# Performance work log

Hardware: AMD Instinct MI355X
Metric: run time of the kernel (lower is better)

Reference implementation:

```python
import jax, jax.numpy as jnp
import numpy as np

D_MODEL = 1024
NUM_HEADS = 16
HEAD_DIM = D_MODEL // NUM_HEADS


def setup_inputs() -> dict:
    key = jax.random.key(0)
    ks = jax.random.split(key, 5)
    scale = 1.0 / np.sqrt(D_MODEL)
    x = jax.random.normal(ks[0], (2, 2048, D_MODEL), dtype=jnp.float32)
    W_qkv = jax.random.normal(ks[1], (D_MODEL, 3 * D_MODEL), dtype=jnp.float32) * scale
    b_qkv = jnp.zeros((3 * D_MODEL,), dtype=jnp.float32)
    W_proj = jax.random.normal(ks[2], (D_MODEL, D_MODEL), dtype=jnp.float32) * scale
    b_proj = jnp.zeros((D_MODEL,), dtype=jnp.float32)
    return {"x": x, "W_qkv": W_qkv, "b_qkv": b_qkv, "W_proj": W_proj, "b_proj": b_proj}


def reference(x, W_qkv, b_qkv, W_proj, b_proj):
    B, S, D = x.shape
    qkv = x @ W_qkv + b_qkv                      # [B,S,3D]
    qkv = qkv.reshape(B, S, 3, NUM_HEADS, HEAD_DIM)
    qkv = jnp.transpose(qkv, (2, 0, 3, 1, 4))    # [3,B,H,S,hd]
    q, k, v = qkv[0], qkv[1], qkv[2]
    scores = jnp.einsum('bhqd,bhkd->bhqk', q, k) / jnp.sqrt(jnp.asarray(HEAD_DIM, x.dtype))
    probs = jax.nn.softmax(scores, axis=-1)
    out = jnp.einsum('bhqk,bhkd->bhqd', probs, v)  # [B,H,S,hd]
    out = jnp.transpose(out, (0, 2, 1, 3)).reshape(B, S, D)
    return out @ W_proj + b_proj
```

## Files before the change

kernel.cpp:

```cpp
#include <hip/hip_runtime.h>
#include <math.h>

#define B_ 2
#define S_ 2048
#define D_ 1024
#define H_ 16
#define HD_ 64

typedef __bf16 bf16x8 __attribute__((ext_vector_type(8)));
typedef __bf16 bf16x4 __attribute__((ext_vector_type(4)));
typedef __bf16 bf16x2 __attribute__((ext_vector_type(2)));
typedef float f32x4 __attribute__((ext_vector_type(4)));
typedef float f32x16 __attribute__((ext_vector_type(16)));
typedef unsigned u32x2 __attribute__((ext_vector_type(2)));

#define GLOAD16(gsrc, ldst) \
  __builtin_amdgcn_global_load_lds((const __attribute__((address_space(1))) void*)(gsrc), \
                                   (__attribute__((address_space(3))) void*)(ldst), 16, 0, 0)

static __device__ __forceinline__ unsigned pack2(float a, float b) {
    bf16x2 v; v[0] = (__bf16)a; v[1] = (__bf16)b;
    return __builtin_bit_cast(unsigned, v);
}

__global__ __launch_bounds__(256) void conv_k(
    const float* __restrict__ in, __bf16* __restrict__ out)
{
    int i = (blockIdx.x * 256 + threadIdx.x) * 8;
    float4 a = *(const float4*)(in + i);
    float4 b = *(const float4*)(in + i + 4);
    bf16x8 v;
    v[0] = (__bf16)a.x; v[1] = (__bf16)a.y; v[2] = (__bf16)a.z; v[3] = (__bf16)a.w;
    v[4] = (__bf16)b.x; v[5] = (__bf16)b.y; v[6] = (__bf16)b.z; v[7] = (__bf16)b.w;
    *(bf16x8*)(out + i) = v;
}

__global__ __launch_bounds__(256) void transpose_bf16_k(
    const float* __restrict__ in, __bf16* __restrict__ t_out, int K, int N)
{
    __shared__ float t[64][65];
    const int tid = threadIdx.x;
    const int bj = blockIdx.x * 64;
    const int bi = blockIdx.y * 64;
    #pragma unroll
    for (int it = 0; it < 4; ++it) {
        int idx = (tid + it * 256) * 4;
        int r = idx >> 6, c = idx & 63;
        float4 v = *(const float4*)(in + (size_t)(bi + r) * N + bj + c);
        t[r][c] = v.x; t[r][c+1] = v.y; t[r][c+2] = v.z; t[r][c+3] = v.w;
    }
    __syncthreads();
    int j = tid & 63;
    int i0 = (tid >> 6) * 16;
    bf16x8 h0, h1;
    #pragma unroll
    for (int ii = 0; ii < 8; ++ii) h0[ii] = (__bf16)t[i0 + ii][j];
    #pragma unroll
    for (int ii = 0; ii < 8; ++ii) h1[ii] = (__bf16)t[i0 + 8 + ii][j];
    size_t o = (size_t)(bj + j) * K + bi + i0;
    *(bf16x8*)(t_out + o) = h0; *(bf16x8*)(t_out + o + 8) = h1;
}

template<typename OutT>
__global__ __launch_bounds__(256) void gemm_nt_k(
    const __bf16* __restrict__ A, const __bf16* __restrict__ Bt,
    const float* __restrict__ bias, OutT* __restrict__ C,
    int M, int N, int K)
{
    constexpr int TSZ = 128 * 64;
    __shared__ __bf16 sA[TSZ];
    __shared__ __bf16 sB[TSZ];

    const int tid = threadIdx.x, w = tid >> 6, l = tid & 63;
    const int lr = l & 15, lg = l >> 4;
    const int bm = blockIdx.y * 128, bn = blockIdx.x * 128;
    const int wm = w >> 1, wn = w & 1;

    f32x4 acc[4][4] = {};

    for (int k0 = 0; k0 < K; k0 += 64) {
        __syncthreads();
        #pragma unroll
        for (int c = 0; c < 4; ++c) {
            int q = w * 4 + c;
            int r = q * 8 + (l >> 3);
            int sl = ((l & 7) ^ (r & 7)) * 8;
            GLOAD16(A + (size_t)(bm + r) * K + k0 + sl, sA + q * 512);
            GLOAD16(Bt + (size_t)(bn + r) * K + k0 + sl, sB + q * 512);
        }
        __syncthreads();
        #pragma unroll
        for (int kk = 0; kk < 2; ++kk) {
            bf16x8 ah[4], bh[4];
            #pragma unroll
            for (int i = 0; i < 4; ++i) {
                int ra = wm * 64 + i * 16 + lr;
                int sa = ((kk * 4 + lg) ^ (ra & 7)) * 8;
                ah[i] = *(const bf16x8*)(sA + ra * 64 + sa);
                int rb = wn * 64 + i * 16 + lr;
                int sb = ((kk * 4 + lg) ^ (rb & 7)) * 8;
                bh[i] = *(const bf16x8*)(sB + rb * 64 + sb);
            }
            #pragma unroll
            for (int mi = 0; mi < 4; ++mi)
                #pragma unroll
                for (int ni = 0; ni < 4; ++ni)
                    acc[mi][ni] = __builtin_amdgcn_mfma_f32_16x16x32_bf16(ah[mi], bh[ni], acc[mi][ni], 0, 0, 0);
        }
    }

    #pragma unroll
    for (int ni = 0; ni < 4; ++ni) {
        int col = bn + wn * 64 + ni * 16 + lr;
        float bv = bias[col];
        #pragma unroll
        for (int mi = 0; mi < 4; ++mi) {
            #pragma unroll
            for (int r = 0; r < 4; ++r) {
                int row = bm + wm * 64 + mi * 16 + lg * 4 + r;
                float v = acc[mi][ni][r] + bv;
                C[(size_t)row * N + col] = (OutT)v;
            }
        }
    }
}

__global__ __launch_bounds__(512) void attn32_k(
    const __bf16* __restrict__ qkv, __bf16* __restrict__ attn)
{
    __shared__ __bf16 Ks[2][64 * 64];
    __shared__ __bf16 Vt[2][64 * 64];

    const int tid = threadIdx.x, w = tid >> 6, l = tid & 63;
    const int q32 = l & 31, hi = l >> 5;
    const int bid = blockIdx.x;
    const int qt = bid >> 5, hb = bid & 31;
    const int h = hb >> 1, b = hb & 1;
    const int q0 = qt * 256;
    const size_t ldq = 3 * D_;
    const __bf16* Qg = qkv + (size_t)b * S_ * ldq + h * HD_;
    const __bf16* Kg = Qg + D_;
    const __bf16* Vg = Qg + 2 * D_;
    const int qg = q0 + w * 32 + q32;

    const float C2  = 0.125f * 1.44269504f;
    const float OFF = 20.0f * 1.44269504f;

    bf16x8 qf[4];
    #pragma unroll
    for (int ds = 0; ds < 4; ++ds)
        qf[ds] = *(const bf16x8*)(Qg + (size_t)qg * ldq + ds * 16 + hi * 8);

    const int krow = tid >> 3;
    const int ksl  = (tid & 7) ^ (krow & 7);
    const int vk   = tid & 63;
    const int vd0  = (tid >> 6) * 8;
    int voff[8];
    #pragma unroll
    for (int j = 0; j < 8; ++j)
        voff[j] = (vd0 + j) * 128 + (((vk >> 3) ^ j) * 16) + (vk & 7) * 2;

    f32x16 o[2] = {};
    float lsum = 0.f;
    bf16x8 vr;

    auto stageK = [&](int kt, int buf) {
        GLOAD16(Kg + (size_t)(kt * 64 + krow) * ldq + ksl * 8, &Ks[buf][w * 512]);
    };
    auto loadV = [&](int kt) {
        vr = *(const bf16x8*)(Vg + (size_t)(kt * 64 + vk) * ldq + vd0);
    };
    auto writeV = [&](int buf) {
        #pragma unroll
        for (int j = 0; j < 8; ++j)
            *(__bf16*)((char*)&Vt[buf][0] + voff[j]) = vr[j];
    };

    stageK(0, 0);
    loadV(0);
    writeV(0);
    __syncthreads();

    constexpr int NT = S_ / 64;
    for (int kt = 0; kt < NT; ++kt) {
        const int cur = kt & 1, nxt = cur ^ 1;
        if (kt < NT - 1) { stageK(kt + 1, nxt); loadV(kt + 1); }

        f32x16 sc[2] = {};
        #pragma unroll
        for (int kb = 0; kb < 2; ++kb) {
            int r = kb * 32 + q32;
            #pragma unroll
            for (int ds = 0; ds < 4; ++ds) {
                int slot = (ds * 2 + hi) ^ (r & 7);
                bf16x8 kf = *(const bf16x8*)((const char*)&Ks[cur][0] + r * 128 + slot * 16);
                sc[kb] = __builtin_amdgcn_mfma_f32_32x32x16_bf16(kf, qf[ds], sc[kb], 0, 0, 0);
            }
        }

        float sum = 0.f;
        #pragma unroll
        for (int kb = 0; kb < 2; ++kb)
            #pragma unroll
            for (int i = 0; i < 16; ++i) {
                float pv = exp2f(fmaf(sc[kb][i], C2, -OFF));
                sc[kb][i] = pv;
                sum += pv;
            }
        lsum += sum;

        bf16x8 pa[2][2];
        #pragma unroll
        for (int kb = 0; kb < 2; ++kb) {
            #pragma unroll
            for (int tl = 0; tl < 2; ++tl) {
                int base = tl * 8;
                unsigned A0 = pack2(sc[kb][base + 0], sc[kb][base + 1]);
                unsigned A1 = pack2(sc[kb][base + 2], sc[kb][base + 3]);
                unsigned B0 = pack2(sc[kb][base + 4], sc[kb][base + 5]);
                unsigned B1 = pack2(sc[kb][base + 6], sc[kb][base + 7]);
                u32x2 s0 = __builtin_amdgcn_permlane32_swap(A0, B0, false, false);
                u32x2 s1 = __builtin_amdgcn_permlane32_swap(A1, B1, false, false);
                union { unsigned u[4]; bf16x8 v; } pu;
                pu.u[0] = s0[0]; pu.u[1] = s1[0]; pu.u[2] = s0[1]; pu.u[3] = s1[1];
                pa[kb][tl] = pu.v;
            }
        }

        #pragma unroll
        for (int db = 0; db < 2; ++db) {
            int dr = db * 32 + q32;
            #pragma unroll
            for (int t = 0; t < 4; ++t) {
                int slot = (t * 2 + hi) ^ (dr & 7);
                bf16x8 vf = *(const bf16x8*)((const char*)&Vt[cur][0] + dr * 128 + slot * 16);
                o[db] = __builtin_amdgcn_mfma_f32_32x32x16_bf16(vf, pa[t >> 1][t & 1], o[db], 0, 0, 0);
            }
        }

        if (kt < NT - 1) writeV(nxt);
        __syncthreads();
    }

    lsum += __shfl_xor(lsum, 32);
    float inv = 1.0f / lsum;
    #pragma unroll
    for (int db = 0; db < 2; ++db)
        #pragma unroll
        for (int rg = 0; rg < 4; ++rg) {
            int d = db * 32 + 8 * rg + 4 * hi;
            bf16x4 ov;
            #pragma unroll
            for (int i = 0; i < 4; ++i) ov[i] = (__bf16)(o[db][rg * 4 + i] * inv);
            *(bf16x4*)(attn + ((size_t)b * S_ + qg) * D_ + h * HD_ + d) = ov;
        }
}

extern "C" void kernel_launch(void* const* d_in, const int* in_sizes, int n_in,
                              void* d_out, int out_size, void* d_ws, size_t ws_size,
                              hipStream_t stream) {
    const float* x     = (const float*)d_in[0];
    const float* Wqkv  = (const float*)d_in[1];
    const float* bqkv  = (const float*)d_in[2];
    const float* Wproj = (const float*)d_in[3];
    const float* bproj = (const float*)d_in[4];

    __bf16* ws = (__bf16*)d_ws;
    const size_t MB = 1024 * 1024 / 2;
    __bf16* x_bf  = ws;
    __bf16* wq_t  = x_bf + 8 * MB;
    __bf16* wp_t  = wq_t + 6 * MB;
    __bf16* qkv   = wp_t + 2 * MB;
    __bf16* attn  = qkv + 24 * MB;

    const int M = B_ * S_;

    conv_k<<<2048, 256, 0, stream>>>(x, x_bf);
    transpose_bf16_k<<<dim3(48, 16), 256, 0, stream>>>(Wqkv, wq_t, D_, 3 * D_);
    transpose_bf16_k<<<dim3(16, 16), 256, 0, stream>>>(Wproj, wp_t, D_, D_);

    gemm_nt_k<__bf16><<<dim3(24, 32), 256, 0, stream>>>(
        x_bf, wq_t, bqkv, qkv, M, 3 * D_, D_);

    attn32_k<<<256, 512, 0, stream>>>(qkv, attn);

    gemm_nt_k<float><<<dim3(8, 32), 256, 0, stream>>>(
        attn, wp_t, bproj, (float*)d_out, M, D_, D_);
}
```

Before: 146.7 us.

## Fold softmax scale into Q weights, halve attention block size, add MFMA priority hints

After: 150.4 us. 1.03x slower.

```diff
diff --git a/kernel.cpp b/kernel.cpp
--- a/kernel.cpp
+++ b/kernel.cpp
@@ -17,6 +17,8 @@
 #define GLOAD16(gsrc, ldst) \
   __builtin_amdgcn_global_load_lds((const __attribute__((address_space(1))) void*)(gsrc), \
                                    (__attribute__((address_space(3))) void*)(ldst), 16, 0, 0)
+
+#define QSCALE 0.18033688f
 
 static __device__ __forceinline__ unsigned pack2(float a, float b) {
     bf16x2 v; v[0] = (__bf16)a; v[1] = (__bf16)b;
@@ -36,7 +38,8 @@
 }
 
 __global__ __launch_bounds__(256) void transpose_bf16_k(
-    const float* __restrict__ in, __bf16* __restrict__ t_out, int K, int N)
+    const float* __restrict__ in, __bf16* __restrict__ t_out, int K, int N,
+    int qcols, float qs)
 {
     __shared__ float t[64][65];
     const int tid = threadIdx.x;
@@ -52,11 +55,12 @@
     __syncthreads();
     int j = tid & 63;
     int i0 = (tid >> 6) * 16;
+    float s = (bj + j) < qcols ? qs : 1.0f;
     bf16x8 h0, h1;
     #pragma unroll
-    for (int ii = 0; ii < 8; ++ii) h0[ii] = (__bf16)t[i0 + ii][j];
-    #pragma unroll
-    for (int ii = 0; ii < 8; ++ii) h1[ii] = (__bf16)t[i0 + 8 + ii][j];
+    for (int ii = 0; ii < 8; ++ii) h0[ii] = (__bf16)(t[i0 + ii][j] * s);
+    #pragma unroll
+    for (int ii = 0; ii < 8; ++ii) h1[ii] = (__bf16)(t[i0 + 8 + ii][j] * s);
     size_t o = (size_t)(bj + j) * K + bi + i0;
     *(bf16x8*)(t_out + o) = h0; *(bf16x8*)(t_out + o + 8) = h1;
 }
@@ -65,7 +69,7 @@
 __global__ __launch_bounds__(256) void gemm_nt_k(
     const __bf16* __restrict__ A, const __bf16* __restrict__ Bt,
     const float* __restrict__ bias, OutT* __restrict__ C,
-    int M, int N, int K)
+    int M, int N, int K, int qcols, float qs)
 {
     constexpr int TSZ = 128 * 64;
     __shared__ __bf16 sA[TSZ];
@@ -113,6 +117,7 @@
     for (int ni = 0; ni < 4; ++ni) {
         int col = bn + wn * 64 + ni * 16 + lr;
         float bv = bias[col];
+        if (col < qcols) bv *= qs;
         #pragma unroll
         for (int mi = 0; mi < 4; ++mi) {
             #pragma unroll
@@ -125,7 +130,7 @@
     }
 }
 
-__global__ __launch_bounds__(512) void attn32_k(
+__global__ __launch_bounds__(256) void attn32_k(
     const __bf16* __restrict__ qkv, __bf16* __restrict__ attn)
 {
     __shared__ __bf16 Ks[2][64 * 64];
@@ -136,44 +141,52 @@
     const int bid = blockIdx.x;
     const int qt = bid >> 5, hb = bid & 31;
     const int h = hb >> 1, b = hb & 1;
-    const int q0 = qt * 256;
+    const int q0 = qt * 128;
     const size_t ldq = 3 * D_;
     const __bf16* Qg = qkv + (size_t)b * S_ * ldq + h * HD_;
     const __bf16* Kg = Qg + D_;
     const __bf16* Vg = Qg + 2 * D_;
     const int qg = q0 + w * 32 + q32;
 
-    const float C2  = 0.125f * 1.44269504f;
-    const float OFF = 20.0f * 1.44269504f;
-
     bf16x8 qf[4];
     #pragma unroll
     for (int ds = 0; ds < 4; ++ds)
         qf[ds] = *(const bf16x8*)(Qg + (size_t)qg * ldq + ds * 16 + hi * 8);
 
-    const int krow = tid >> 3;
-    const int ksl  = (tid & 7) ^ (krow & 7);
-    const int vk   = tid & 63;
-    const int vd0  = (tid >> 6) * 8;
-    int voff[8];
-    #pragma unroll
-    for (int j = 0; j < 8; ++j)
-        voff[j] = (vd0 + j) * 128 + (((vk >> 3) ^ j) * 16) + (vk & 7) * 2;
+    int krow[2], ksl[2], voff[2][8];
+    const int vk = l;
+    #pragma unroll
+    for (int c = 0; c < 2; ++c) {
+        int p = (w * 2 + c) * 64 + l;
+        krow[c] = p >> 3;
+        ksl[c]  = (p & 7) ^ (krow[c] & 7);
+        int d0 = (w * 2 + c) * 8;
+        #pragma unroll
+        for (int j = 0; j < 8; ++j)
+            voff[c][j] = (d0 + j) * 128 + (((vk >> 3) ^ j) * 16) + (vk & 7) * 2;
+    }
 
     f32x16 o[2] = {};
     float lsum = 0.f;
-    bf16x8 vr;
+    bf16x8 vr[2];
 
     auto stageK = [&](int kt, int buf) {
-        GLOAD16(Kg + (size_t)(kt * 64 + krow) * ldq + ksl * 8, &Ks[buf][w * 512]);
+        #pragma unroll
+        for (int c = 0; c < 2; ++c)
+            GLOAD16(Kg + (size_t)(kt * 64 + krow[c]) * ldq + ksl[c] * 8,
+                    &Ks[buf][(w * 2 + c) * 512]);
     };
     auto loadV = [&](int kt) {
-        vr = *(const bf16x8*)(Vg + (size_t)(kt * 64 + vk) * ldq + vd0);
+        #pragma unroll
+        for (int c = 0; c < 2; ++c)
+            vr[c] = *(const bf16x8*)(Vg + (size_t)(kt * 64 + vk) * ldq + (w * 2 + c) * 8);
     };
     auto writeV = [&](int buf) {
         #pragma unroll
-        for (int j = 0; j < 8; ++j)
-            *(__bf16*)((char*)&Vt[buf][0] + voff[j]) = vr[j];
+        for (int c = 0; c < 2; ++c)
+            #pragma unroll
+            for (int j = 0; j < 8; ++j)
+                *(__bf16*)((char*)&Vt[buf][0] + voff[c][j]) = vr[c][j];
     };
 
     stageK(0, 0);
@@ -187,6 +200,7 @@
         if (kt < NT - 1) { stageK(kt + 1, nxt); loadV(kt + 1); }
 
         f32x16 sc[2] = {};
+        __builtin_amdgcn_s_setprio(1);
         #pragma unroll
         for (int kb = 0; kb < 2; ++kb) {
             int r = kb * 32 + q32;
@@ -197,13 +211,14 @@
                 sc[kb] = __builtin_amdgcn_mfma_f32_32x32x16_bf16(kf, qf[ds], sc[kb], 0, 0, 0);
             }
         }
+        __builtin_amdgcn_s_setprio(0);
 
         float sum = 0.f;
         #pragma unroll
         for (int kb = 0; kb < 2; ++kb)
             #pragma unroll
             for (int i = 0; i < 16; ++i) {
-                float pv = exp2f(fmaf(sc[kb][i], C2, -OFF));
+                float pv = exp2f(sc[kb][i]);
                 sc[kb][i] = pv;
                 sum += pv;
             }
@@ -227,6 +242,7 @@
             }
         }
 
+        __builtin_amdgcn_s_setprio(1);
         #pragma unroll
         for (int db = 0; db < 2; ++db) {
             int dr = db * 32 + q32;
@@ -237,6 +253,7 @@
                 o[db] = __builtin_amdgcn_mfma_f32_32x32x16_bf16(vf, pa[t >> 1][t & 1], o[db], 0, 0, 0);
             }
         }
+        __builtin_amdgcn_s_setprio(0);
 
         if (kt < NT - 1) writeV(nxt);
         __syncthreads();
@@ -276,14 +293,14 @@
     const int M = B_ * S_;
 
     conv_k<<<2048, 256, 0, stream>>>(x, x_bf);
-    transpose_bf16_k<<<dim3(48, 16), 256, 0, stream>>>(Wqkv, wq_t, D_, 3 * D_);
-    transpose_bf16_k<<<dim3(16, 16), 256, 0, stream>>>(Wproj, wp_t, D_, D_);
+    transpose_bf16_k<<<dim3(48, 16), 256, 0, stream>>>(Wqkv, wq_t, D_, 3 * D_, D_, QSCALE);
+    transpose_bf16_k<<<dim3(16, 16), 256, 0, stream>>>(Wproj, wp_t, D_, D_, 0, 1.0f);
 
     gemm_nt_k<__bf16><<<dim3(24, 32), 256, 0, stream>>>(
-        x_bf, wq_t, bqkv, qkv, M, 3 * D_, D_);
-
-    attn32_k<<<256, 512, 0, stream>>>(qkv, attn);
+        x_bf, wq_t, bqkv, qkv, M, 3 * D_, D_, D_, QSCALE);
+
+    attn32_k<<<512, 256, 0, stream>>>(qkv, attn);
 
     gemm_nt_k<float><<<dim3(8, 32), 256, 0, stream>>>(
-        attn, wp_t, bproj, (float*)d_out, M, D_, D_);
-}
+        attn, wp_t, bproj, (float*)d_out, M, D_, D_, 0, 1.0f);
+}
```
